# Kernel optimization log

Hardware: AMD Instinct MI355X
Metric: run time of the kernel (lower is better)

Reference implementation:

```python
import jax, jax.numpy as jnp
import numpy as np

EPS = 1e-12  # F.normalize default eps

def _l2norm(x, axis):
    n = jnp.sqrt(jnp.sum(x * x, axis=axis, keepdims=True))
    return x / jnp.maximum(n, EPS)

def setup_inputs() -> dict:
    key = jax.random.key(0)
    ks = jax.random.split(key, 6)
    N, C, K, B, OUT = 200000, 256, 64, 8, 1024
    alpha = 100.0
    feat = jax.random.normal(ks[0], (N, C), dtype=jnp.float32)
    batch_ids = jax.random.randint(ks[1], (N,), 0, B, dtype=jnp.int32)
    centroids = jax.random.uniform(ks[2], (K, C), dtype=jnp.float32)
    # _init_params: conv weight = 2*alpha*centroids, bias = -alpha*||centroid||_2
    conv_w = 2.0 * alpha * centroids
    conv_b = -alpha * jnp.sqrt(jnp.sum(centroids * centroids, axis=1))
    fc_w = jax.random.normal(ks[3], (OUT, K * C), dtype=jnp.float32) * (1.0 / np.sqrt(K * C))
    fc_b = jax.random.normal(ks[4], (OUT,), dtype=jnp.float32) * 0.01
    return {"feat": feat, "batch_ids": batch_ids, "centroids": centroids,
            "conv_w": conv_w, "conv_b": conv_b, "fc_w": fc_w, "fc_b": fc_b,
            "batch_size": B}

def reference(feat, batch_ids, centroids, conv_w, conv_b, fc_w, fc_b, batch_size):
    B = int(batch_size)
    K, C = centroids.shape
    # descriptor-wise L2 normalization (normalize_input=True)
    x = _l2norm(feat, axis=1)                       # [N, C]
    # 1x1 conv == linear: soft assignment logits per point
    logits = x @ conv_w.T + conv_b                  # [N, K]
    soft = jax.nn.softmax(logits, axis=1)           # [N, K]
    # Per-batch aggregation (replaces the python loop):
    # vlad[b,k,:] = sum_{p in b} soft[p,k] * x[p,:] - (sum_{p in b} soft[p,k]) * centroids[k,:]
    onehot = jax.nn.one_hot(batch_ids, B, dtype=x.dtype)          # [N, B]
    A = jnp.einsum('nb,nk,nc->bkc', onehot, soft, x)              # [B, K, C]
    S = jax.ops.segment_sum(soft, batch_ids, num_segments=B)      # [B, K]
    vlad = A - S[:, :, None] * centroids[None, :, :]              # [B, K, C]
    vlad = _l2norm(vlad, axis=2)                                  # intra-normalization over C
    v = vlad.reshape(B, K * C)
    out = v @ fc_w.T + fc_b                                       # [B, 1024]
    return _l2norm(out, axis=1)
```

## Files before the change

### kernel.cpp

```cpp
#include <hip/hip_runtime.h>
#include <hip/hip_bf16.h>

typedef __attribute__((ext_vector_type(8))) short bf16x8;
typedef __attribute__((ext_vector_type(4))) float f32x4;

#define PCAP 768

__global__ void p0_wsplit(const float* __restrict__ convw,
                          short* __restrict__ whi, short* __restrict__ wlo)
{
    int e = blockIdx.x * 256 + threadIdx.x;
    if (e >= 2048) return;
    int lane = e & 63;
    int kstep = (e >> 6) & 7;
    int nt = e >> 9;
    int cluster = nt * 16 + (lane & 15);
    int ch0 = kstep * 32 + (lane >> 4) * 8;
    const float* src = convw + cluster * 256 + ch0;
    #pragma unroll
    for (int j = 0; j < 8; ++j) {
        float x = src[j];
        unsigned u = __float_as_uint(x);
        unsigned uh = u & 0xffff0000u;
        float r = x - __uint_as_float(uh);
        whi[e * 8 + j] = (short)(u >> 16);
        wlo[e * 8 + j] = (short)(__float_as_uint(r) >> 16);
    }
}

__global__ __launch_bounds__(256) void p1_mfma(
    const float* __restrict__ feat, const int* __restrict__ bids,
    const short* __restrict__ whi, const short* __restrict__ wlo,
    const float* __restrict__ convb,
    float* __restrict__ soft, float* __restrict__ invn, int* __restrict__ cnts, int N)
{
    __shared__ float ssq_lds[64];
    __shared__ int cnt[8];
    const int t = threadIdx.x;
    if (t < 8) cnt[t] = 0;
    const int w = t >> 6, lane = t & 63;
    const int m = lane & 15, quad = lane >> 4;
    const int p0 = blockIdx.x * 64;
    const int gp = p0 + w * 16 + m;
    const bool valid = gp < N;

    f32x4 acc[4];
    #pragma unroll
    for (int nt = 0; nt < 4; ++nt) acc[nt] = (f32x4){0.f, 0.f, 0.f, 0.f};
    float ssq = 0.f;

    const float* frow = feat + (size_t)gp * 256 + quad * 8;
    const bf16x8* WH = (const bf16x8*)whi;
    const bf16x8* WL = (const bf16x8*)wlo;

    for (int ks = 0; ks < 8; ++ks) {
        float x[8];
        if (valid) {
            float4 v0 = *(const float4*)(frow + ks * 32);
            float4 v1 = *(const float4*)(frow + ks * 32 + 4);
            x[0] = v0.x; x[1] = v0.y; x[2] = v0.z; x[3] = v0.w;
            x[4] = v1.x; x[5] = v1.y; x[6] = v1.z; x[7] = v1.w;
        } else {
            #pragma unroll
            for (int j = 0; j < 8; ++j) x[j] = 0.f;
        }
        bf16x8 ahi, alo;
        #pragma unroll
        for (int j = 0; j < 8; ++j) {
            unsigned u = __float_as_uint(x[j]);
            unsigned uh = u & 0xffff0000u;
            float r = x[j] - __uint_as_float(uh);
            ahi[j] = (short)(u >> 16);
            alo[j] = (short)(__float_as_uint(r) >> 16);
            ssq += x[j] * x[j];
        }
        #pragma unroll
        for (int nt = 0; nt < 4; ++nt) {
            bf16x8 bhi = WH[(nt * 8 + ks) * 64 + lane];
            bf16x8 blo = WL[(nt * 8 + ks) * 64 + lane];
            acc[nt] = __builtin_amdgcn_mfma_f32_16x16x32_bf16(ahi, bhi, acc[nt], 0, 0, 0);
            acc[nt] = __builtin_amdgcn_mfma_f32_16x16x32_bf16(ahi, blo, acc[nt], 0, 0, 0);
            acc[nt] = __builtin_amdgcn_mfma_f32_16x16x32_bf16(alo, bhi, acc[nt], 0, 0, 0);
        }
    }

    ssq += __shfl_xor(ssq, 16);
    ssq += __shfl_xor(ssq, 32);
    if (quad == 0) ssq_lds[w * 16 + m] = ssq;
    __syncthreads();

    float bias[4];
    #pragma unroll
    for (int nt = 0; nt < 4; ++nt) bias[nt] = convb[nt * 16 + m];

    #pragma unroll
    for (int r = 0; r < 4; ++r) {
        int pl = quad * 4 + r;
        int gpt = p0 + w * 16 + pl;
        float inv = rsqrtf(fmaxf(ssq_lds[w * 16 + pl], 1e-24f));
        float v[4];
        #pragma unroll
        for (int nt = 0; nt < 4; ++nt) v[nt] = acc[nt][r] * inv + bias[nt];
        float mx = fmaxf(fmaxf(v[0], v[1]), fmaxf(v[2], v[3]));
        #pragma unroll
        for (int off = 8; off >= 1; off >>= 1) mx = fmaxf(mx, __shfl_xor(mx, off));
        float e[4];
        float s = 0.f;
        #pragma unroll
        for (int nt = 0; nt < 4; ++nt) { e[nt] = __expf(v[nt] - mx); s += e[nt]; }
        #pragma unroll
        for (int off = 8; off >= 1; off >>= 1) s += __shfl_xor(s, off);
        float rs = 1.0f / s;
        if (gpt < N) {
            #pragma unroll
            for (int nt = 0; nt < 4; ++nt)
                soft[(size_t)gpt * 64 + nt * 16 + m] = e[nt] * rs;
            if (m == 0) {
                invn[gpt] = inv;
                atomicAdd(&cnt[bids[gpt]], 1);
            }
        }
    }
    __syncthreads();
    if (t < 8) atomicAdd(&cnts[t], cnt[t]);
}

__global__ void p2_offsets(const int* __restrict__ cnts, int* __restrict__ offs, int* __restrict__ cur)
{
    if (threadIdx.x == 0) {
        int acc = 0;
        for (int b = 0; b < 8; ++b) { offs[b] = acc; cur[b] = acc; acc += cnts[b]; }
        offs[8] = acc;
    }
}

__global__ __launch_bounds__(256) void p2_scatter(
    const int* __restrict__ bids, int* __restrict__ cur, int* __restrict__ perm, int N)
{
    __shared__ int lcnt[8], lbase[8];
    const int t = threadIdx.x;
    if (t < 8) lcnt[t] = 0;
    __syncthreads();
    int p = blockIdx.x * 256 + t;
    int b = 0, my = 0;
    bool ok = p < N;
    if (ok) { b = bids[p]; my = atomicAdd(&lcnt[b], 1); }
    __syncthreads();
    if (t < 8) lbase[t] = atomicAdd(&cur[t], lcnt[t]);
    __syncthreads();
    if (ok) perm[lbase[b] + my] = p;
}

__global__ __launch_bounds__(256) void p3_mfma(
    const float* __restrict__ feat, const float* __restrict__ soft,
    const float* __restrict__ invn, const int* __restrict__ perm,
    const int* __restrict__ offs, float* __restrict__ partial,
    float* __restrict__ S, int split)
{
    __shared__ short xsT_hi[256 * 32];
    __shared__ short xsT_lo[256 * 32];
    __shared__ short sT_hi[64 * 32];
    __shared__ short sT_lo[64 * 32];
    __shared__ int   pidxL[PCAP];
    __shared__ float invL[PCAP];

    const int b  = blockIdx.x / split;
    const int sp = blockIdx.x % split;
    const int start = offs[b], end = offs[b + 1];
    const int len = end - start;
    const int chunk = (len + split - 1) / split;
    const int s0 = start + sp * chunk;
    int myLen = end - s0;
    myLen = max(0, min(myLen, chunk));
    myLen = min(myLen, PCAP);

    const int t = threadIdx.x;
    const int w = t >> 6, lane = t & 63;
    const int m = lane & 15, quad = lane >> 4;

    for (int i = t; i < myLen; i += 256) pidxL[i] = perm[s0 + i];
    __syncthreads();
    for (int i = t; i < myLen; i += 256) invL[i] = invn[pidxL[i]];
    __syncthreads();

    f32x4 acc[16];
    #pragma unroll
    for (int ct = 0; ct < 16; ++ct) acc[ct] = (f32x4){0.f, 0.f, 0.f, 0.f};
    float sacc = 0.f;

    const int nch = (myLen + 31) >> 5;
    for (int q = 0; q < nch; ++q) {
        const int p0 = q * 32;
        int pids[8];
        float pinv[8];
        #pragma unroll
        for (int j = 0; j < 8; ++j) {
            int pl = p0 + w * 8 + j;
            bool ok = pl < myLen;
            pids[j] = ok ? pidxL[pl] : -1;
            pinv[j] = ok ? invL[pl] : 0.f;
        }
        #pragma unroll
        for (int cg = 0; cg < 4; ++cg) {
            int c = cg * 64 + lane;
            float vals[8];
            #pragma unroll
            for (int j = 0; j < 8; ++j) {
                float v = 0.f;
                if (pids[j] >= 0) v = feat[(size_t)pids[j] * 256 + c] * pinv[j];
                vals[j] = v;
            }
            bf16x8 vh, vl;
            #pragma unroll
            for (int j = 0; j < 8; ++j) {
                unsigned u = __float_as_uint(vals[j]);
                float r = vals[j] - __uint_as_float(u & 0xffff0000u);
                vh[j] = (short)(u >> 16);
                vl[j] = (short)(__float_as_uint(r) >> 16);
            }
            *(bf16x8*)&xsT_hi[c * 32 + w * 8] = vh;
            *(bf16x8*)&xsT_lo[c * 32 + w * 8] = vl;
        }
        {
            float svals[8];
            #pragma unroll
            for (int j = 0; j < 8; ++j) {
                float v = 0.f;
                if (pids[j] >= 0) v = soft[(size_t)pids[j] * 64 + lane];
                svals[j] = v;
                sacc += v;
            }
            bf16x8 vh, vl;
            #pragma unroll
            for (int j = 0; j < 8; ++j) {
                unsigned u = __float_as_uint(svals[j]);
                float r = svals[j] - __uint_as_float(u & 0xffff0000u);
                vh[j] = (short)(u >> 16);
                vl[j] = (short)(__float_as_uint(r) >> 16);
            }
            *(bf16x8*)&sT_hi[lane * 32 + w * 8] = vh;
            *(bf16x8*)&sT_lo[lane * 32 + w * 8] = vl;
        }
        __syncthreads();
        bf16x8 ah = *(const bf16x8*)&sT_hi[(w * 16 + m) * 32 + quad * 8];
        bf16x8 al = *(const bf16x8*)&sT_lo[(w * 16 + m) * 32 + quad * 8];
        #pragma unroll
        for (int ct = 0; ct < 16; ++ct) {
            bf16x8 bh = *(const bf16x8*)&xsT_hi[(ct * 16 + m) * 32 + quad * 8];
            bf16x8 bl = *(const bf16x8*)&xsT_lo[(ct * 16 + m) * 32 + quad * 8];
            acc[ct] = __builtin_amdgcn_mfma_f32_16x16x32_bf16(ah, bh, acc[ct], 0, 0, 0);
            acc[ct] = __builtin_amdgcn_mfma_f32_16x16x32_bf16(ah, bl, acc[ct], 0, 0, 0);
            acc[ct] = __builtin_amdgcn_mfma_f32_16x16x32_bf16(al, bh, acc[ct], 0, 0, 0);
        }
        __syncthreads();
    }

    float* dst = partial + (size_t)(b * split + sp) * 64 * 256;
    #pragma unroll
    for (int ct = 0; ct < 16; ++ct) {
        #pragma unroll
        for (int r = 0; r < 4; ++r) {
            int k = w * 16 + quad * 4 + r;
            dst[k * 256 + ct * 16 + m] = acc[ct][r];
        }
    }
    atomicAdd(S + b * 64 + lane, sacc);
}

__global__ __launch_bounds__(256) void p4a_vlad(
    const float* __restrict__ partial, const float* __restrict__ S,
    const float* __restrict__ cents, float* __restrict__ v, int split)
{
    const int b = blockIdx.x >> 6, k = blockIdx.x & 63;
    const int t = threadIdx.x;
    float sum = 0.f;
    const float* base = partial + ((size_t)(b * split) * 64 + k) * 256 + t;
    for (int sp = 0; sp < split; ++sp)
        sum += base[(size_t)sp * 64 * 256];
    float val = sum - S[b * 64 + k] * cents[k * 256 + t];
    float sq = val * val;
    #pragma unroll
    for (int off = 32; off >= 1; off >>= 1) sq += __shfl_xor(sq, off);
    __shared__ float wsum[4];
    if ((t & 63) == 0) wsum[t >> 6] = sq;
    __syncthreads();
    float tot = wsum[0] + wsum[1] + wsum[2] + wsum[3];
    float r = 1.0f / fmaxf(sqrtf(tot), 1e-12f);
    v[b * 16384 + k * 256 + t] = val * r;
}

__global__ __launch_bounds__(256) void p4b_fc(
    const float* __restrict__ v, const float* __restrict__ fcw,
    const float* __restrict__ fcb, float* __restrict__ pre)
{
    const int t = threadIdx.x;
    const int o0 = blockIdx.x * 4;
    float acc[4][8] = {};
    for (int it = 0; it < 64; ++it) {
        int i = it * 256 + t;
        float wv[4];
        #pragma unroll
        for (int oo = 0; oo < 4; ++oo) wv[oo] = fcw[(size_t)(o0 + oo) * 16384 + i];
        #pragma unroll
        for (int b = 0; b < 8; ++b) {
            float vv = v[b * 16384 + i];
            #pragma unroll
            for (int oo = 0; oo < 4; ++oo) acc[oo][b] += wv[oo] * vv;
        }
    }
    __shared__ float red[32][4];
    #pragma unroll
    for (int oo = 0; oo < 4; ++oo)
        #pragma unroll
        for (int b = 0; b < 8; ++b) {
            float sv = acc[oo][b];
            #pragma unroll
            for (int off = 32; off >= 1; off >>= 1) sv += __shfl_xor(sv, off);
            if ((t & 63) == 0) red[oo * 8 + b][t >> 6] = sv;
        }
    __syncthreads();
    if (t < 32) {
        int oo = t >> 3, b = t & 7;
        float sv = red[t][0] + red[t][1] + red[t][2] + red[t][3];
        pre[b * 1024 + o0 + oo] = sv + fcb[o0 + oo];
    }
}

__global__ __launch_bounds__(256) void p5_norm(const float* __restrict__ pre, float* __restrict__ out)
{
    const int b = blockIdx.x, t = threadIdx.x;
    float vals[4];
    float sq = 0.f;
    #pragma unroll
    for (int i = 0; i < 4; ++i) {
        vals[i] = pre[b * 1024 + t + 256 * i];
        sq += vals[i] * vals[i];
    }
    #pragma unroll
    for (int off = 32; off >= 1; off >>= 1) sq += __shfl_xor(sq, off);
    __shared__ float wsum[4];
    if ((t & 63) == 0) wsum[t >> 6] = sq;
    __syncthreads();
    float tot = wsum[0] + wsum[1] + wsum[2] + wsum[3];
    float r = 1.0f / fmaxf(sqrtf(tot), 1e-12f);
    #pragma unroll
    for (int i = 0; i < 4; ++i) out[b * 1024 + t + 256 * i] = vals[i] * r;
}

extern "C" void kernel_launch(void* const* d_in, const int* in_sizes, int n_in,
                              void* d_out, int out_size, void* d_ws, size_t ws_size,
                              hipStream_t stream)
{
    const float* feat  = (const float*)d_in[0];
    const int*   bids  = (const int*)d_in[1];
    const float* cents = (const float*)d_in[2];
    const float* convw = (const float*)d_in[3];
    const float* convb = (const float*)d_in[4];
    const float* fcw   = (const float*)d_in[5];
    const float* fcb   = (const float*)d_in[6];
    float* out = (float*)d_out;

    const int N = in_sizes[0] / 256;

    const size_t base_floats = 16384
                             + (size_t)N * 64  + N
                             + 512  + 8 * 16384  + 8192 ;
    const size_t base_ints = (size_t)N + 8 + 9 + 8;
    int split = 96;
    while (split > 16) {
        size_t tot = (base_floats + (size_t)split * 8 * 16384) * 4 + base_ints * 4;
        if (tot <= ws_size) break;
        split -= 16;
    }

    short* whi = (short*)d_ws;
    short* wlo = whi + 16384;
    float* soft = (float*)(wlo + 16384);
    float* invn = soft + (size_t)N * 64;
    float* partial = invn + N;
    float* S    = partial + (size_t)split * 8 * 16384;
    float* v    = S + 512;
    float* pre  = v + 8 * 16384;
    int* perm = (int*)(pre + 8192);
    int* cnts = perm + N;
    int* offs = cnts + 8;
    int* cur  = offs + 9;

    hipMemsetAsync(S, 0, 512 * sizeof(float), stream);
    hipMemsetAsync(cnts, 0, 8 * sizeof(int), stream);

    p0_wsplit<<<8, 256, 0, stream>>>(convw, whi, wlo);
    p1_mfma<<<(N + 63) / 64, 256, 0, stream>>>(feat, bids, whi, wlo, convb, soft, invn, cnts, N);
    p2_offsets<<<1, 64, 0, stream>>>(cnts, offs, cur);
    p2_scatter<<<(N + 255) / 256, 256, 0, stream>>>(bids, cur, perm, N);
    p3_mfma<<<8 * split, 256, 0, stream>>>(feat, soft, invn, perm, offs, partial, S, split);
    p4a_vlad<<<512, 256, 0, stream>>>(partial, S, cents, v, split);
    p4b_fc<<<256, 256, 0, stream>>>(v, fcw, fcb, pre);
    p5_norm<<<8, 256, 0, stream>>>(pre, out);
}
```

Measured before the change: 571.5 us.

## Fuse soft-assignment GEMM and softmax into the per-batch VLAD aggregation kernel

Moves the logits GEMM, L2 norm and softmax into the aggregation kernel, which now reads each feature row once through the permutation. Soft weights and inverse norms stay in registers and LDS instead of a global round trip, and the separate p1 pass over feat is gone. Batch counts now come from a lightweight count kernel. It also removes the PCAP cap on points per block and lowers split from 96 to 64. In exchange there is heavy register pressure (64-entry xint array plus 16 accumulators) and more LDS traffic per iteration.

```diff
diff --git a/kernel.cpp b/kernel.cpp
--- a/kernel.cpp
+++ b/kernel.cpp
@@ -4,7 +4,7 @@
 typedef __attribute__((ext_vector_type(8))) short bf16x8;
 typedef __attribute__((ext_vector_type(4))) float f32x4;
 
-#define PCAP 768
+#define XT_STRIDE 72
 
 __global__ void p0_wsplit(const float* __restrict__ convw,
                           short* __restrict__ whi, short* __restrict__ wlo)
@@ -28,99 +28,15 @@
     }
 }
 
-__global__ __launch_bounds__(256) void p1_mfma(
-    const float* __restrict__ feat, const int* __restrict__ bids,
-    const short* __restrict__ whi, const short* __restrict__ wlo,
-    const float* __restrict__ convb,
-    float* __restrict__ soft, float* __restrict__ invn, int* __restrict__ cnts, int N)
-{
-    __shared__ float ssq_lds[64];
+__global__ __launch_bounds__(256) void p2_count(const int* __restrict__ bids,
+                                                int* __restrict__ cnts, int N)
+{
     __shared__ int cnt[8];
     const int t = threadIdx.x;
     if (t < 8) cnt[t] = 0;
-    const int w = t >> 6, lane = t & 63;
-    const int m = lane & 15, quad = lane >> 4;
-    const int p0 = blockIdx.x * 64;
-    const int gp = p0 + w * 16 + m;
-    const bool valid = gp < N;
-
-    f32x4 acc[4];
-    #pragma unroll
-    for (int nt = 0; nt < 4; ++nt) acc[nt] = (f32x4){0.f, 0.f, 0.f, 0.f};
-    float ssq = 0.f;
-
-    const float* frow = feat + (size_t)gp * 256 + quad * 8;
-    const bf16x8* WH = (const bf16x8*)whi;
-    const bf16x8* WL = (const bf16x8*)wlo;
-
-    for (int ks = 0; ks < 8; ++ks) {
-        float x[8];
-        if (valid) {
-            float4 v0 = *(const float4*)(frow + ks * 32);
-            float4 v1 = *(const float4*)(frow + ks * 32 + 4);
-            x[0] = v0.x; x[1] = v0.y; x[2] = v0.z; x[3] = v0.w;
-            x[4] = v1.x; x[5] = v1.y; x[6] = v1.z; x[7] = v1.w;
-        } else {
-            #pragma unroll
-            for (int j = 0; j < 8; ++j) x[j] = 0.f;
-        }
-        bf16x8 ahi, alo;
-        #pragma unroll
-        for (int j = 0; j < 8; ++j) {
-            unsigned u = __float_as_uint(x[j]);
-            unsigned uh = u & 0xffff0000u;
-            float r = x[j] - __uint_as_float(uh);
-            ahi[j] = (short)(u >> 16);
-            alo[j] = (short)(__float_as_uint(r) >> 16);
-            ssq += x[j] * x[j];
-        }
-        #pragma unroll
-        for (int nt = 0; nt < 4; ++nt) {
-            bf16x8 bhi = WH[(nt * 8 + ks) * 64 + lane];
-            bf16x8 blo = WL[(nt * 8 + ks) * 64 + lane];
-            acc[nt] = __builtin_amdgcn_mfma_f32_16x16x32_bf16(ahi, bhi, acc[nt], 0, 0, 0);
-            acc[nt] = __builtin_amdgcn_mfma_f32_16x16x32_bf16(ahi, blo, acc[nt], 0, 0, 0);
-            acc[nt] = __builtin_amdgcn_mfma_f32_16x16x32_bf16(alo, bhi, acc[nt], 0, 0, 0);
-        }
-    }
-
-    ssq += __shfl_xor(ssq, 16);
-    ssq += __shfl_xor(ssq, 32);
-    if (quad == 0) ssq_lds[w * 16 + m] = ssq;
-    __syncthreads();
-
-    float bias[4];
-    #pragma unroll
-    for (int nt = 0; nt < 4; ++nt) bias[nt] = convb[nt * 16 + m];
-
-    #pragma unroll
-    for (int r = 0; r < 4; ++r) {
-        int pl = quad * 4 + r;
-        int gpt = p0 + w * 16 + pl;
-        float inv = rsqrtf(fmaxf(ssq_lds[w * 16 + pl], 1e-24f));
-        float v[4];
-        #pragma unroll
-        for (int nt = 0; nt < 4; ++nt) v[nt] = acc[nt][r] * inv + bias[nt];
-        float mx = fmaxf(fmaxf(v[0], v[1]), fmaxf(v[2], v[3]));
-        #pragma unroll
-        for (int off = 8; off >= 1; off >>= 1) mx = fmaxf(mx, __shfl_xor(mx, off));
-        float e[4];
-        float s = 0.f;
-        #pragma unroll
-        for (int nt = 0; nt < 4; ++nt) { e[nt] = __expf(v[nt] - mx); s += e[nt]; }
-        #pragma unroll
-        for (int off = 8; off >= 1; off >>= 1) s += __shfl_xor(s, off);
-        float rs = 1.0f / s;
-        if (gpt < N) {
-            #pragma unroll
-            for (int nt = 0; nt < 4; ++nt)
-                soft[(size_t)gpt * 64 + nt * 16 + m] = e[nt] * rs;
-            if (m == 0) {
-                invn[gpt] = inv;
-                atomicAdd(&cnt[bids[gpt]], 1);
-            }
-        }
-    }
+    __syncthreads();
+    int p = blockIdx.x * 256 + t;
+    if (p < N) atomicAdd(&cnt[bids[p]], 1);
     __syncthreads();
     if (t < 8) atomicAdd(&cnts[t], cnt[t]);
 }
@@ -151,18 +67,15 @@
     if (ok) perm[lbase[b] + my] = p;
 }
 
-__global__ __launch_bounds__(256) void p3_mfma(
-    const float* __restrict__ feat, const float* __restrict__ soft,
-    const float* __restrict__ invn, const int* __restrict__ perm,
-    const int* __restrict__ offs, float* __restrict__ partial,
-    float* __restrict__ S, int split)
-{
-    __shared__ short xsT_hi[256 * 32];
-    __shared__ short xsT_lo[256 * 32];
-    __shared__ short sT_hi[64 * 32];
-    __shared__ short sT_lo[64 * 32];
-    __shared__ int   pidxL[PCAP];
-    __shared__ float invL[PCAP];
+__global__ __launch_bounds__(256, 2) void fused13(
+    const float* __restrict__ feat,
+    const short* __restrict__ whi, const short* __restrict__ wlo,
+    const float* __restrict__ convb,
+    const int* __restrict__ perm, const int* __restrict__ offs,
+    float* __restrict__ partial, float* __restrict__ S, int split)
+{
+    __shared__ unsigned xT[128 * XT_STRIDE];
+    __shared__ unsigned sT[64 * XT_STRIDE];
 
     const int b  = blockIdx.x / split;
     const int sp = blockIdx.x % split;
@@ -170,101 +83,162 @@
     const int len = end - start;
     const int chunk = (len + split - 1) / split;
     const int s0 = start + sp * chunk;
-    int myLen = end - s0;
-    myLen = max(0, min(myLen, chunk));
-    myLen = min(myLen, PCAP);
+    int myLen = min(chunk, end - s0);
+    if (myLen < 0) myLen = 0;
 
     const int t = threadIdx.x;
     const int w = t >> 6, lane = t & 63;
     const int m = lane & 15, quad = lane >> 4;
 
-    for (int i = t; i < myLen; i += 256) pidxL[i] = perm[s0 + i];
-    __syncthreads();
-    for (int i = t; i < myLen; i += 256) invL[i] = invn[pidxL[i]];
-    __syncthreads();
-
-    f32x4 acc[16];
-    #pragma unroll
-    for (int ct = 0; ct < 16; ++ct) acc[ct] = (f32x4){0.f, 0.f, 0.f, 0.f};
-    float sacc = 0.f;
-
-    const int nch = (myLen + 31) >> 5;
-    for (int q = 0; q < nch; ++q) {
-        const int p0 = q * 32;
-        int pids[8];
-        float pinv[8];
-        #pragma unroll
-        for (int j = 0; j < 8; ++j) {
-            int pl = p0 + w * 8 + j;
-            bool ok = pl < myLen;
-            pids[j] = ok ? pidxL[pl] : -1;
-            pinv[j] = ok ? invL[pl] : 0.f;
-        }
-        #pragma unroll
-        for (int cg = 0; cg < 4; ++cg) {
-            int c = cg * 64 + lane;
-            float vals[8];
+    const bf16x8* WH = (const bf16x8*)whi;
+    const bf16x8* WL = (const bf16x8*)wlo;
+
+    float bias[4];
+    #pragma unroll
+    for (int nt = 0; nt < 4; ++nt) bias[nt] = convb[nt * 16 + m];
+
+    f32x4 acc2[16];
+    #pragma unroll
+    for (int ct = 0; ct < 16; ++ct) acc2[ct] = (f32x4){0.f, 0.f, 0.f, 0.f};
+    float saccv[4] = {0.f, 0.f, 0.f, 0.f};
+
+    const int nIter = (myLen + 63) >> 6;
+    for (int it = 0; it < nIter; ++it) {
+        const int pl = it * 64 + w * 16 + m;
+        const int pid = (pl < myLen) ? perm[s0 + pl] : -1;
+        const bool valid = pid >= 0;
+        const float* frow = feat + (size_t)pid * 256 + quad * 8;
+
+        f32x4 acc1[4];
+        #pragma unroll
+        for (int nt = 0; nt < 4; ++nt) acc1[nt] = (f32x4){0.f, 0.f, 0.f, 0.f};
+        float ssq = 0.f;
+        unsigned xint[64];
+
+        #pragma unroll
+        for (int ks = 0; ks < 8; ++ks) {
+            float x[8];
+            if (valid) {
+                float4 v0 = *(const float4*)(frow + ks * 32);
+                float4 v1 = *(const float4*)(frow + ks * 32 + 4);
+                x[0] = v0.x; x[1] = v0.y; x[2] = v0.z; x[3] = v0.w;
+                x[4] = v1.x; x[5] = v1.y; x[6] = v1.z; x[7] = v1.w;
+            } else {
+                #pragma unroll
+                for (int j = 0; j < 8; ++j) x[j] = 0.f;
+            }
+            bf16x8 ahi, alo;
             #pragma unroll
             for (int j = 0; j < 8; ++j) {
-                float v = 0.f;
-                if (pids[j] >= 0) v = feat[(size_t)pids[j] * 256 + c] * pinv[j];
-                vals[j] = v;
-            }
-            bf16x8 vh, vl;
-            #pragma unroll
-            for (int j = 0; j < 8; ++j) {
-                unsigned u = __float_as_uint(vals[j]);
-                float r = vals[j] - __uint_as_float(u & 0xffff0000u);
-                vh[j] = (short)(u >> 16);
-                vl[j] = (short)(__float_as_uint(r) >> 16);
-            }
-            *(bf16x8*)&xsT_hi[c * 32 + w * 8] = vh;
-            *(bf16x8*)&xsT_lo[c * 32 + w * 8] = vl;
-        }
-        {
-            float svals[8];
-            #pragma unroll
-            for (int j = 0; j < 8; ++j) {
-                float v = 0.f;
-                if (pids[j] >= 0) v = soft[(size_t)pids[j] * 64 + lane];
-                svals[j] = v;
-                sacc += v;
-            }
-            bf16x8 vh, vl;
-            #pragma unroll
-            for (int j = 0; j < 8; ++j) {
-                unsigned u = __float_as_uint(svals[j]);
-                float r = svals[j] - __uint_as_float(u & 0xffff0000u);
-                vh[j] = (short)(u >> 16);
-                vl[j] = (short)(__float_as_uint(r) >> 16);
-            }
-            *(bf16x8*)&sT_hi[lane * 32 + w * 8] = vh;
-            *(bf16x8*)&sT_lo[lane * 32 + w * 8] = vl;
-        }
-        __syncthreads();
-        bf16x8 ah = *(const bf16x8*)&sT_hi[(w * 16 + m) * 32 + quad * 8];
-        bf16x8 al = *(const bf16x8*)&sT_lo[(w * 16 + m) * 32 + quad * 8];
-        #pragma unroll
-        for (int ct = 0; ct < 16; ++ct) {
-            bf16x8 bh = *(const bf16x8*)&xsT_hi[(ct * 16 + m) * 32 + quad * 8];
-            bf16x8 bl = *(const bf16x8*)&xsT_lo[(ct * 16 + m) * 32 + quad * 8];
-            acc[ct] = __builtin_amdgcn_mfma_f32_16x16x32_bf16(ah, bh, acc[ct], 0, 0, 0);
-            acc[ct] = __builtin_amdgcn_mfma_f32_16x16x32_bf16(ah, bl, acc[ct], 0, 0, 0);
-            acc[ct] = __builtin_amdgcn_mfma_f32_16x16x32_bf16(al, bh, acc[ct], 0, 0, 0);
-        }
-        __syncthreads();
+                unsigned u = __float_as_uint(x[j]);
+                float r = x[j] - __uint_as_float(u & 0xffff0000u);
+                unsigned lo = __float_as_uint(r) >> 16;
+                ahi[j] = (short)(u >> 16);
+                alo[j] = (short)lo;
+                xint[ks * 8 + j] = (u & 0xffff0000u) | lo;
+                ssq += x[j] * x[j];
+            }
+            #pragma unroll
+            for (int nt = 0; nt < 4; ++nt) {
+                bf16x8 bhi = WH[(nt * 8 + ks) * 64 + lane];
+                bf16x8 blo = WL[(nt * 8 + ks) * 64 + lane];
+                acc1[nt] = __builtin_amdgcn_mfma_f32_16x16x32_bf16(ahi, bhi, acc1[nt], 0, 0, 0);
+                acc1[nt] = __builtin_amdgcn_mfma_f32_16x16x32_bf16(ahi, blo, acc1[nt], 0, 0, 0);
+                acc1[nt] = __builtin_amdgcn_mfma_f32_16x16x32_bf16(alo, bhi, acc1[nt], 0, 0, 0);
+            }
+        }
+        ssq += __shfl_xor(ssq, 16);
+        ssq += __shfl_xor(ssq, 32);
+
+        #pragma unroll
+        for (int r = 0; r < 4; ++r) {
+            int prow = quad * 4 + r;
+            int plp = it * 64 + w * 16 + prow;
+            bool pv = plp < myLen;
+            float psq = __shfl(ssq, (lane & 48) | prow);
+            float inv = rsqrtf(fmaxf(psq, 1e-24f));
+            float v[4];
+            #pragma unroll
+            for (int nt = 0; nt < 4; ++nt) v[nt] = acc1[nt][r] * inv + bias[nt];
+            float mx = fmaxf(fmaxf(v[0], v[1]), fmaxf(v[2], v[3]));
+            #pragma unroll
+            for (int off = 8; off >= 1; off >>= 1) mx = fmaxf(mx, __shfl_xor(mx, off));
+            float e[4]; float s = 0.f;
+            #pragma unroll
+            for (int nt = 0; nt < 4; ++nt) { e[nt] = __expf(v[nt] - mx); s += e[nt]; }
+            #pragma unroll
+            for (int off = 8; off >= 1; off >>= 1) s += __shfl_xor(s, off);
+            float rs = 1.0f / s;
+            #pragma unroll
+            for (int nt = 0; nt < 4; ++nt) {
+                float so = pv ? e[nt] * rs : 0.f;
+                saccv[nt] += so;
+                float sos = so * inv;
+                unsigned u = __float_as_uint(sos);
+                float rr = sos - __uint_as_float(u & 0xffff0000u);
+                unsigned pk = (u & 0xffff0000u) | (__float_as_uint(rr) >> 16);
+                sT[(nt * 16 + m) * XT_STRIDE + w * 16 + prow] = pk;
+            }
+        }
+
+        #pragma unroll
+        for (int h = 0; h < 2; ++h) {
+            #pragma unroll
+            for (int kk = 0; kk < 4; ++kk) {
+                #pragma unroll
+                for (int j = 0; j < 8; ++j) {
+                    int cr = kk * 32 + quad * 8 + j;
+                    xT[cr * XT_STRIDE + w * 16 + m] = xint[(h * 4 + kk) * 8 + j];
+                }
+            }
+            __syncthreads();
+            bf16x8 ah[2], al[2];
+            #pragma unroll
+            for (int ks2 = 0; ks2 < 2; ++ks2) {
+                const unsigned* ap = &sT[(w * 16 + m) * XT_STRIDE + ks2 * 32 + quad * 8];
+                #pragma unroll
+                for (int j = 0; j < 8; ++j) {
+                    unsigned pk = ap[j];
+                    ah[ks2][j] = (short)(pk >> 16);
+                    al[ks2][j] = (short)(pk & 0xffffu);
+                }
+            }
+            #pragma unroll
+            for (int ctl = 0; ctl < 8; ++ctl) {
+                const int ct = h * 8 + ctl;
+                #pragma unroll
+                for (int ks2 = 0; ks2 < 2; ++ks2) {
+                    const unsigned* bp = &xT[(ctl * 16 + m) * XT_STRIDE + ks2 * 32 + quad * 8];
+                    bf16x8 bh, bl;
+                    #pragma unroll
+                    for (int j = 0; j < 8; ++j) {
+                        unsigned pk = bp[j];
+                        bh[j] = (short)(pk >> 16);
+                        bl[j] = (short)(pk & 0xffffu);
+                    }
+                    acc2[ct] = __builtin_amdgcn_mfma_f32_16x16x32_bf16(ah[ks2], bh, acc2[ct], 0, 0, 0);
+                    acc2[ct] = __builtin_amdgcn_mfma_f32_16x16x32_bf16(ah[ks2], bl, acc2[ct], 0, 0, 0);
+                    acc2[ct] = __builtin_amdgcn_mfma_f32_16x16x32_bf16(al[ks2], bh, acc2[ct], 0, 0, 0);
+                }
+            }
+            __syncthreads();
+        }
     }
 
     float* dst = partial + (size_t)(b * split + sp) * 64 * 256;
     #pragma unroll
-    for (int ct = 0; ct < 16; ++ct) {
-        #pragma unroll
-        for (int r = 0; r < 4; ++r) {
-            int k = w * 16 + quad * 4 + r;
-            dst[k * 256 + ct * 16 + m] = acc[ct][r];
-        }
-    }
-    atomicAdd(S + b * 64 + lane, sacc);
+    for (int ct = 0; ct < 16; ++ct)
+        #pragma unroll
+        for (int r = 0; r < 4; ++r)
+            dst[(w * 16 + quad * 4 + r) * 256 + ct * 16 + m] = acc2[ct][r];
+
+    #pragma unroll
+    for (int nt = 0; nt < 4; ++nt) {
+        float sv = saccv[nt];
+        sv += __shfl_xor(sv, 16);
+        sv += __shfl_xor(sv, 32);
+        if (quad == 0) atomicAdd(S + b * 64 + nt * 16 + m, sv);
+    }
 }
 
 __global__ __launch_bounds__(256) void p4a_vlad(
@@ -362,11 +336,10 @@
 
     const int N = in_sizes[0] / 256;
 
-    const size_t base_floats = 16384
-                             + (size_t)N * 64  + N
-                             + 512  + 8 * 16384  + 8192 ;
+    const size_t base_floats = 16384  + 512
+                             + 8 * 16384  + 8192 ;
     const size_t base_ints = (size_t)N + 8 + 9 + 8;
-    int split = 96;
+    int split = 64;
     while (split > 16) {
         size_t tot = (base_floats + (size_t)split * 8 * 16384) * 4 + base_ints * 4;
         if (tot <= ws_size) break;
@@ -375,9 +348,7 @@
 
     short* whi = (short*)d_ws;
     short* wlo = whi + 16384;
-    float* soft = (float*)(wlo + 16384);
-    float* invn = soft + (size_t)N * 64;
-    float* partial = invn + N;
+    float* partial = (float*)(wlo + 16384);
     float* S    = partial + (size_t)split * 8 * 16384;
     float* v    = S + 512;
     float* pre  = v + 8 * 16384;
@@ -390,10 +361,10 @@
     hipMemsetAsync(cnts, 0, 8 * sizeof(int), stream);
 
     p0_wsplit<<<8, 256, 0, stream>>>(convw, whi, wlo);
-    p1_mfma<<<(N + 63) / 64, 256, 0, stream>>>(feat, bids, whi, wlo, convb, soft, invn, cnts, N);
+    p2_count<<<(N + 255) / 256, 256, 0, stream>>>(bids, cnts, N);
     p2_offsets<<<1, 64, 0, stream>>>(cnts, offs, cur);
     p2_scatter<<<(N + 255) / 256, 256, 0, stream>>>(bids, cur, perm, N);
-    p3_mfma<<<8 * split, 256, 0, stream>>>(feat, soft, invn, perm, offs, partial, S, split);
+    fused13<<<8 * split, 256, 0, stream>>>(feat, whi, wlo, convb, perm, offs, partial, S, split);
     p4a_vlad<<<512, 256, 0, stream>>>(partial, S, cents, v, split);
     p4b_fc<<<256, 256, 0, stream>>>(v, fcw, fcb, pre);
     p5_norm<<<8, 256, 0, stream>>>(pre, out);
```

After: 659.1 us. 15.3% more time.
